# Optimization experiments

Measured on AMD Instinct MI355X. Metric: run time of the kernel, lower is better.

The kernel has to match this reference:

```python
import jax, jax.numpy as jnp
import numpy as np
import math

B_, V_, D_, N_, H_, W_ = 4, 8, 64, 16, 32, 32
V_LIST = [0.0, 45.0, 90.0, 135.0, 180.0, 225.0, 270.0, 315.0]
GROUPS = 4
EPS = 1e-5


def _make_sample_coords():
    # Replicates F.affine_grid(align_corners=False) for fixed rotation matrices,
    # then maps normalized grid coords to input pixel coords as grid_sample does.
    xs = (np.arange(W_) + 0.5) * 2.0 / W_ - 1.0
    ys = (np.arange(H_) + 0.5) * 2.0 / H_ - 1.0
    X, Y = np.meshgrid(xs, ys)  # (H, W)
    ix_list, iy_list = [], []
    for w in V_LIST:
        a = math.radians(-w)
        c, s = math.cos(a), math.sin(a)
        gx = c * X - s * Y  # theta = [[c,-s,0],[s,c,0]]
        gy = s * X + c * Y
        ix_list.append((gx + 1.0) * W_ / 2.0 - 0.5)
        iy_list.append((gy + 1.0) * H_ / 2.0 - 0.5)
    return (jnp.asarray(np.stack(ix_list), jnp.float32),
            jnp.asarray(np.stack(iy_list), jnp.float32))

IX, IY = _make_sample_coords()  # each (V, H, W)


def _bilinear(sv, iy, ix):
    # sv: (B, D, N, H, W); iy, ix: (H, W) float sampling coords (pixel space)
    x0 = jnp.floor(ix)
    y0 = jnp.floor(iy)
    wx1 = ix - x0
    wy1 = iy - y0

    def corner(yc, xc, wgt):
        m = (yc >= 0) & (yc < H_) & (xc >= 0) & (xc < W_)  # zeros padding
        yi = jnp.clip(yc, 0, H_ - 1).astype(jnp.int32)
        xi = jnp.clip(xc, 0, W_ - 1).astype(jnp.int32)
        return sv[..., yi, xi] * jnp.where(m, wgt, 0.0)

    return (corner(y0, x0, (1.0 - wy1) * (1.0 - wx1))
            + corner(y0, x0 + 1.0, (1.0 - wy1) * wx1)
            + corner(y0 + 1.0, x0, wy1 * (1.0 - wx1))
            + corner(y0 + 1.0, x0 + 1.0, wy1 * wx1))

# vmap over the velocity axis V of s_prev and the per-velocity grids
_transport = jax.vmap(_bilinear, in_axes=(1, 0, 0), out_axes=1)


def _conv(x, w, b=None):
    y = jax.lax.conv_general_dilated(x, w, (1, 1), 'SAME',
                                     dimension_numbers=('NCHW', 'OIHW', 'NCHW'))
    if b is not None:
        y = y + b[None, :, None, None]
    return y


def _group_norm(x, w, b):
    Bn, D, H, W = x.shape
    xg = x.reshape(Bn, GROUPS, D // GROUPS, H, W)
    mu = xg.mean(axis=(2, 3, 4), keepdims=True)
    var = xg.var(axis=(2, 3, 4), keepdims=True)
    xn = ((xg - mu) * jax.lax.rsqrt(var + EPS)).reshape(Bn, D, H, W)
    return xn * w[None, :, None, None] + b[None, :, None, None]


def setup_inputs() -> dict:
    key = jax.random.key(0)
    ks = jax.random.split(key, 5)
    return {
        "u_t": jax.random.normal(ks[0], (B_, D_, H_, W_), jnp.float32),
        "s_prev": jax.random.normal(ks[1], (B_, V_, D_, N_, H_, W_), jnp.float32) * 0.1,
        "gn_w": jnp.ones((D_,), jnp.float32),
        "gn_b": jnp.zeros((D_,), jnp.float32),
        "conv_delta_w": jax.random.normal(ks[2], (D_, D_, 3, 3), jnp.float32) * 0.02,
        "conv_delta_b": jnp.zeros((D_,), jnp.float32),
        "conv_B_w": jax.random.normal(ks[3], (N_, D_, 3, 3), jnp.float32) * 0.02,
        "conv_C_w": jax.random.normal(ks[4], (N_, D_, 3, 3), jnp.float32) * 0.02,
        "log_A_real": jnp.full((D_, N_), math.log(0.5), jnp.float32),
        "D_param": jnp.ones((D_,), jnp.float32),
        "dt_bias": jnp.float32(math.log(math.e - 1.0)),
    }


def reference(u_t, s_prev, gn_w, gn_b, conv_delta_w, conv_delta_b,
              conv_B_w, conv_C_w, log_A_real, D_param, dt_bias):
    u_norm = _group_norm(u_t, gn_w, gn_b)
    delta = jax.nn.softplus(_conv(u_norm, conv_delta_w, conv_delta_b) + dt_bias)
    delta = jnp.clip(delta, 1e-4, 5.0)                               # (B,D,H,W)
    B_val = _conv(u_norm, conv_B_w)                                  # (B,N,H,W)
    C_val = _conv(u_norm, conv_C_w)                                  # (B,N,H,W)
    A = -jnp.exp(log_A_real)                                         # (D,N)
    A_bar = jnp.exp(delta[:, :, None] * A[None, :, :, None, None])   # (B,D,N,H,W)
    B_bar = delta[:, :, None] * B_val[:, None]                       # (B,D,N,H,W)
    s_trans = _transport(s_prev, IY, IX)                             # (B,V,D,N,H,W)
    s_new = A_bar[:, None] * s_trans + B_bar[:, None] * u_t[:, None, :, None]
    y_state = jnp.einsum('bvdnhw,bnhw->bvdhw', s_new, C_val)
    y_new = y_state + u_t[:, None] * D_param[None, None, :, None, None]
    return (y_new, s_new)
```

## Files before the change

kernel.cpp:

```cpp
#include <hip/hip_runtime.h>
#include <cmath>

#define FSQ 0.70710678118654752440f
__constant__ float CTAB[8] = {1.f,  FSQ, 0.f, -FSQ, -1.f, -FSQ, 0.f, FSQ};
__constant__ float STAB[8] = {0.f, -FSQ, -1.f, -FSQ,  0.f,  FSQ, 1.f, FSQ};

__global__ __launch_bounds__(256) void gn_kernel(const float* __restrict__ u,
                                                 const float* __restrict__ gw,
                                                 const float* __restrict__ gb,
                                                 float* __restrict__ up)
{
    int blk = blockIdx.x;
    int b = blk >> 2, g = blk & 3;
    int t = threadIdx.x;
    const float* src = u + ((size_t)(b * 64 + g * 16) << 10);
    float sum = 0.f, sq = 0.f;
    #pragma unroll
    for (int r = 0; r < 64; ++r) {
        float v = src[t + (r << 8)];
        sum += v; sq += v * v;
    }
    __shared__ float red[256], red2[256];
    red[t] = sum; red2[t] = sq;
    __syncthreads();
    for (int ofs = 128; ofs > 0; ofs >>= 1) {
        if (t < ofs) { red[t] += red[t + ofs]; red2[t] += red2[t + ofs]; }
        __syncthreads();
    }
    float mu  = red[0] * (1.f / 16384.f);
    float var = red2[0] * (1.f / 16384.f) - mu * mu;
    float rs  = rsqrtf(var + 1e-5f);

    float* pb = up + (size_t)(b * 64 + g * 16) * 1156;
    for (int k = t; k < 16 * 132; k += 256) {
        int pl = k / 132, c = k % 132;
        int idx;
        if (c < 34)       idx = c;
        else if (c < 68)  idx = 33 * 34 + (c - 34);
        else if (c < 100) idx = (c - 68 + 1) * 34;
        else              idx = (c - 100 + 1) * 34 + 33;
        pb[pl * 1156 + idx] = 0.f;
    }
    for (int r = 0; r < 64; ++r) {
        int idx = t + (r << 8);
        int ch = idx >> 10, rem = idx & 1023;
        int y = rem >> 5, x = rem & 31;
        float val = (src[idx] - mu) * rs * gw[g * 16 + ch] + gb[g * 16 + ch];
        pb[ch * 1156 + (y + 1) * 34 + (x + 1)] = val;
    }
}

__global__ __launch_bounds__(256) void conv_kernel(const float* __restrict__ up,
                                                   const float* __restrict__ wd,
                                                   const float* __restrict__ bd,
                                                   const float* __restrict__ wB,
                                                   const float* __restrict__ wC,
                                                   const float* __restrict__ dtb,
                                                   float* __restrict__ delta,
                                                   float* __restrict__ Bv,
                                                   float* __restrict__ Cv)
{
    __shared__ float sin_[64 * 204];
    __shared__ float red[256];
    int blk = blockIdx.x;
    int strip = blk & 7;
    int o = (blk >> 3) & 127; o = o % 96;
    o = ((blk >> 3) - (blk / 768) * 96);
    int b = blk / 768;
    int h0 = strip * 4;
    int t = threadIdx.x;

    const float* plane = up + (size_t)b * 73984;
    for (int idx = t; idx < 13056; idx += 256) {
        int ci = idx / 204;
        int rem = idx - ci * 204;
        sin_[idx] = plane[ci * 1156 + h0 * 34 + rem];
    }
    __syncthreads();

    const float* wsel;
    if (o < 64)      wsel = wd + (size_t)o * 576;
    else if (o < 80) wsel = wB + (size_t)(o - 64) * 576;
    else             wsel = wC + (size_t)(o - 80) * 576;

    int half = t >> 7;
    int px = t & 127;
    int r = px >> 5, c = px & 31;
    const float* base = sin_ + r * 34 + c;

    float acc = 0.f;
    int ci0 = half * 32;
    for (int ci = ci0; ci < ci0 + 32; ++ci) {
        const float* pp = base + ci * 204;
        const float* wp = wsel + ci * 9;
        #pragma unroll
        for (int dy = 0; dy < 3; ++dy)
            #pragma unroll
            for (int dx = 0; dx < 3; ++dx)
                acc += pp[dy * 34 + dx] * wp[dy * 3 + dx];
    }
    red[t] = acc;
    __syncthreads();
    if (t < 128) {
        float a = red[t] + red[t + 128];
        int pidx = (h0 + r) * 32 + c;
        if (o < 64) {
            float x = a + bd[o] + dtb[0];
            float sp = (x > 20.f) ? x : log1pf(expf(x));
            sp = fminf(fmaxf(sp, 1e-4f), 5.f);
            delta[((size_t)(b * 64 + o) << 10) + pidx] = sp;
        } else if (o < 80) {
            Bv[((size_t)(b * 16 + o - 64) << 10) + pidx] = a;
        } else {
            Cv[((size_t)(b * 16 + o - 80) << 10) + pidx] = a;
        }
    }
}

__global__ __launch_bounds__(256) void fused_state_kernel(
    const float* __restrict__ s_prev, const float* __restrict__ u_t,
    const float* __restrict__ delta, const float* __restrict__ Bv,
    const float* __restrict__ Cv, const float* __restrict__ logA,
    const float* __restrict__ Dp, float* __restrict__ y_out,
    float* __restrict__ s_out)
{
    __shared__ float lds[8 * 1156];
    __shared__ float Ash[8];
    int blk = blockIdx.x;
    int cchunk = blk & 1;
    int d = (blk >> 1) & 63, v = (blk >> 7) & 7, b = blk >> 10;
    int t = threadIdx.x;

    if (t < 8) Ash[t] = -__expf(logA[d * 16 + cchunk * 8 + t]);
    for (int k = t; k < 1056; k += 256) {
        int pl = k >> 7; int g = k & 127;
        pl = k / 132; g = k - pl * 132;
        int idx;
        if (g < 34)       idx = g;
        else if (g < 68)  idx = 1122 + (g - 34);
        else if (g < 100) idx = (g - 67) * 34;
        else              idx = (g - 99) * 34 + 33;
        lds[pl * 1156 + idx] = 0.f;
    }

    size_t so = (((size_t)((b * 8 + v) * 64 + d)) << 14) + (cchunk << 13);
    const float4* src = (const float4*)(s_prev + so);
    #pragma unroll
    for (int k = 0; k < 8; ++k) {
        int q = t + (k << 8);
        float4 val = src[q];
        int lin = q << 2;
        int nn = lin >> 10, rem = lin & 1023;
        int di = nn * 1156 + ((rem >> 5) + 1) * 34 + (rem & 31) + 1;
        lds[di] = val.x; lds[di + 1] = val.y; lds[di + 2] = val.z; lds[di + 3] = val.w;
    }
    __syncthreads();

    const float cc = CTAB[v], ss = STAB[v];
    const float* dpl = delta + ((size_t)(b * 64 + d) << 10);
    const float* upl = u_t   + ((size_t)(b * 64 + d) << 10);
    const float* bvc = Bv + ((size_t)b << 14) + (cchunk << 13);
    const float* cvc = Cv + ((size_t)b << 14) + (cchunk << 13);
    float* soc = s_out + so;
    float* yo  = y_out + (((size_t)((b * 8 + v) * 64 + d)) << 10);
    float Dd = Dp[d];

    for (int i = 0; i < 4; ++i) {
        int p = t + (i << 8);
        int h = p >> 5, wpx = p & 31;
        float X = (wpx + 0.5f) * 0.0625f - 1.f;
        float Y = (h + 0.5f) * 0.0625f - 1.f;
        float gx = cc * X - ss * Y;
        float gy = ss * X + cc * Y;
        float ix = (gx + 1.f) * 16.f - 0.5f;
        float iy = (gy + 1.f) * 16.f - 0.5f;
        float fx0 = floorf(ix), fy0 = floorf(iy);
        float wx = ix - fx0, wy = iy - fy0;
        int x0 = (int)fx0, y0 = (int)fy0;
        float mx0 = (x0 >= 0 && x0 < 32) ? (1.f - wx) : 0.f;
        float mx1 = (x0 >= -1 && x0 < 31) ? wx : 0.f;
        float my0 = (y0 >= 0 && y0 < 32) ? (1.f - wy) : 0.f;
        float my1 = (y0 >= -1 && y0 < 31) ? wy : 0.f;
        float w00 = my0 * mx0, w01 = my0 * mx1;
        float w10 = my1 * mx0, w11 = my1 * mx1;
        int bx = min(max(x0, -1), 31), by = min(max(y0, -1), 31);
        int base = (by + 1) * 34 + (bx + 1);

        float dd = dpl[p], uv = upl[p];
        float du = dd * uv;
        float yacc = 0.f;
        #pragma unroll
        for (int nn = 0; nn < 8; ++nn) {
            int si = base + nn * 1156;
            float s00 = lds[si], s01 = lds[si + 1];
            float s10 = lds[si + 34], s11 = lds[si + 35];
            float bil = s00 * w00 + s01 * w01 + s10 * w10 + s11 * w11;
            float abar = __expf(dd * Ash[nn]);
            float bvv = bvc[(nn << 10) + p];
            float sn = abar * bil + du * bvv;
            soc[(nn << 10) + p] = sn;
            yacc += sn * cvc[(nn << 10) + p];
        }
        float val = yacc + (cchunk == 0 ? uv * Dd : 0.f);
        atomicAdd(yo + p, val);
    }
}

extern "C" void kernel_launch(void* const* d_in, const int* in_sizes, int n_in,
                              void* d_out, int out_size, void* d_ws, size_t ws_size,
                              hipStream_t stream)
{
    const float* u_t    = (const float*)d_in[0];
    const float* s_prev = (const float*)d_in[1];
    const float* gn_w   = (const float*)d_in[2];
    const float* gn_b   = (const float*)d_in[3];
    const float* wd     = (const float*)d_in[4];
    const float* bd     = (const float*)d_in[5];
    const float* wB     = (const float*)d_in[6];
    const float* wC     = (const float*)d_in[7];
    const float* logA   = (const float*)d_in[8];
    const float* Dp     = (const float*)d_in[9];
    const float* dtb    = (const float*)d_in[10];

    float* y_out = (float*)d_out;
    float* s_out = y_out + 2097152;

    float* up    = (float*)d_ws;
    float* delta = up + 295936;
    float* Bv    = delta + 262144;
    float* Cv    = Bv + 65536;

    hipMemsetAsync(y_out, 0, (size_t)2097152 * sizeof(float), stream);

    hipLaunchKernelGGL(gn_kernel, dim3(16), dim3(256), 0, stream, u_t, gn_w, gn_b, up);
    hipLaunchKernelGGL(conv_kernel, dim3(3072), dim3(256), 0, stream,
                       up, wd, bd, wB, wC, dtb, delta, Bv, Cv);
    hipLaunchKernelGGL(fused_state_kernel, dim3(4096), dim3(256), 0, stream,
                       s_prev, u_t, delta, Bv, Cv, logA, Dp, y_out, s_out);
}
```

Before: 319.3 us.

## Specialize transport for right-angle rotations, drop atomics and memset

The fused state kernel now handles all 16 state channels per block, so y is written directly with float4 stores instead of atomicAdd, and the output memset is removed. Rotations by 0 and 180 degrees read s_prev straight from global memory with index remapping, skipping LDS staging. Rotations by 90 and 270 degrees use a single exact gather instead of bilinear interpolation. Odd-angle views keep bilinear sampling, process 4 pixels per thread and stage two 8-channel chunks through LDS. The costs are more register pressure and branch specialisation per view, and the right-angle paths rely on the fixed angle list being exact.

```diff
diff --git a/kernel.cpp b/kernel.cpp
--- a/kernel.cpp
+++ b/kernel.cpp
@@ -64,9 +64,8 @@
     __shared__ float red[256];
     int blk = blockIdx.x;
     int strip = blk & 7;
-    int o = (blk >> 3) & 127; o = o % 96;
-    o = ((blk >> 3) - (blk / 768) * 96);
     int b = blk / 768;
+    int o = (blk >> 3) - b * 96;
     int h0 = strip * 4;
     int t = threadIdx.x;
 
@@ -125,85 +124,148 @@
     float* __restrict__ s_out)
 {
     __shared__ float lds[8 * 1156];
-    __shared__ float Ash[8];
+    __shared__ float Ash[16];
     int blk = blockIdx.x;
-    int cchunk = blk & 1;
-    int d = (blk >> 1) & 63, v = (blk >> 7) & 7, b = blk >> 10;
+    int d = blk & 63, v = (blk >> 6) & 7, b = blk >> 9;
     int t = threadIdx.x;
 
-    if (t < 8) Ash[t] = -__expf(logA[d * 16 + cchunk * 8 + t]);
-    for (int k = t; k < 1056; k += 256) {
-        int pl = k >> 7; int g = k & 127;
-        pl = k / 132; g = k - pl * 132;
-        int idx;
-        if (g < 34)       idx = g;
-        else if (g < 68)  idx = 1122 + (g - 34);
-        else if (g < 100) idx = (g - 67) * 34;
-        else              idx = (g - 99) * 34 + 33;
-        lds[pl * 1156 + idx] = 0.f;
-    }
-
-    size_t so = (((size_t)((b * 8 + v) * 64 + d)) << 14) + (cchunk << 13);
-    const float4* src = (const float4*)(s_prev + so);
-    #pragma unroll
-    for (int k = 0; k < 8; ++k) {
-        int q = t + (k << 8);
-        float4 val = src[q];
-        int lin = q << 2;
-        int nn = lin >> 10, rem = lin & 1023;
-        int di = nn * 1156 + ((rem >> 5) + 1) * 34 + (rem & 31) + 1;
-        lds[di] = val.x; lds[di + 1] = val.y; lds[di + 2] = val.z; lds[di + 3] = val.w;
+    int h = t >> 3;
+    int x = (t & 7) << 2;
+
+    if (t < 16) Ash[t] = -__expf(logA[d * 16 + t]);
+
+    bool is_odd = (v & 1);
+    if (is_odd) {
+        for (int k = t; k < 1056; k += 256) {
+            int pl = k / 132, g = k - pl * 132;
+            int idx;
+            if (g < 34)       idx = g;
+            else if (g < 68)  idx = 1122 + (g - 34);
+            else if (g < 100) idx = (g - 67) * 34;
+            else              idx = (g - 99) * 34 + 33;
+            lds[pl * 1156 + idx] = 0.f;
+        }
     }
     __syncthreads();
 
-    const float cc = CTAB[v], ss = STAB[v];
-    const float* dpl = delta + ((size_t)(b * 64 + d) << 10);
-    const float* upl = u_t   + ((size_t)(b * 64 + d) << 10);
-    const float* bvc = Bv + ((size_t)b << 14) + (cchunk << 13);
-    const float* cvc = Cv + ((size_t)b << 14) + (cchunk << 13);
-    float* soc = s_out + so;
-    float* yo  = y_out + (((size_t)((b * 8 + v) * 64 + d)) << 10);
+    size_t so = ((size_t)((b * 8 + v) * 64 + d)) << 14;
+    const float*  sb   = s_prev + so;
+    float*        sob  = s_out + so;
+    const float4* dpl4 = (const float4*)(delta + ((size_t)(b * 64 + d) << 10));
+    const float4* upl4 = (const float4*)(u_t   + ((size_t)(b * 64 + d) << 10));
+    const float4* Bv4  = (const float4*)(Bv + ((size_t)b << 14));
+    const float4* Cv4  = (const float4*)(Cv + ((size_t)b << 14));
+    float4*       sot4 = (float4*)sob;
+    float4*       yo4  = (float4*)(y_out + (((size_t)((b * 8 + v) * 64 + d)) << 10));
+
+    float4 dl = dpl4[t];
+    float4 uu = upl4[t];
+    float4 du = make_float4(dl.x * uu.x, dl.y * uu.y, dl.z * uu.z, dl.w * uu.w);
+    float4 yacc = make_float4(0.f, 0.f, 0.f, 0.f);
+
+    if (v == 0 || v == 4) {
+        const float4* sp4 = (const float4*)sb;
+        int rd = (v == 0) ? t : (((31 - h) << 3) + ((28 - x) >> 2));
+        #pragma unroll
+        for (int nn = 0; nn < 16; ++nn) {
+            float4 sp = sp4[(nn << 8) + rd];
+            float s0, s1, s2, s3;
+            if (v == 0) { s0 = sp.x; s1 = sp.y; s2 = sp.z; s3 = sp.w; }
+            else        { s0 = sp.w; s1 = sp.z; s2 = sp.y; s3 = sp.x; }
+            float A = Ash[nn];
+            float4 bv = Bv4[(nn << 8) + t];
+            float4 cv = Cv4[(nn << 8) + t];
+            float4 sn;
+            sn.x = __expf(dl.x * A) * s0 + du.x * bv.x;
+            sn.y = __expf(dl.y * A) * s1 + du.y * bv.y;
+            sn.z = __expf(dl.z * A) * s2 + du.z * bv.z;
+            sn.w = __expf(dl.w * A) * s3 + du.w * bv.w;
+            sot4[(nn << 8) + t] = sn;
+            yacc.x += sn.x * cv.x; yacc.y += sn.y * cv.y;
+            yacc.z += sn.z * cv.z; yacc.w += sn.w * cv.w;
+        }
+    } else {
+        int base0[4];
+        float w00[4], w01[4], w10[4], w11[4];
+        if (is_odd) {
+            const float cc = CTAB[v], ss = STAB[v];
+            #pragma unroll
+            for (int j = 0; j < 4; ++j) {
+                float X = (x + j + 0.5f) * 0.0625f - 1.f;
+                float Y = (h + 0.5f) * 0.0625f - 1.f;
+                float gx = cc * X - ss * Y;
+                float gy = ss * X + cc * Y;
+                float ix = (gx + 1.f) * 16.f - 0.5f;
+                float iy = (gy + 1.f) * 16.f - 0.5f;
+                float fx0 = floorf(ix), fy0 = floorf(iy);
+                float wx = ix - fx0, wy = iy - fy0;
+                int x0 = (int)fx0, y0 = (int)fy0;
+                float mx0 = (x0 >= 0 && x0 < 32) ? (1.f - wx) : 0.f;
+                float mx1 = (x0 >= -1 && x0 < 31) ? wx : 0.f;
+                float my0 = (y0 >= 0 && y0 < 32) ? (1.f - wy) : 0.f;
+                float my1 = (y0 >= -1 && y0 < 31) ? wy : 0.f;
+                w00[j] = my0 * mx0; w01[j] = my0 * mx1;
+                w10[j] = my1 * mx0; w11[j] = my1 * mx1;
+                int bx = min(max(x0, -1), 31), by = min(max(y0, -1), 31);
+                base0[j] = (by + 1) * 34 + (bx + 1);
+            }
+        } else {
+            #pragma unroll
+            for (int j = 0; j < 4; ++j) {
+                if (v == 2) base0[j] = (32 - x - j) * 34 + (h + 1);
+                else        base0[j] = (x + j + 1) * 34 + (32 - h);
+            }
+        }
+
+        for (int ch = 0; ch < 2; ++ch) {
+            const float* src = sb + (ch << 13);
+            #pragma unroll
+            for (int k = 0; k < 32; ++k) {
+                int idx = t + (k << 8);
+                int nn = idx >> 10, rem = idx & 1023;
+                lds[nn * 1156 + ((rem >> 5) + 1) * 34 + (rem & 31) + 1] = src[idx];
+            }
+            __syncthreads();
+
+            #pragma unroll
+            for (int n = 0; n < 8; ++n) {
+                int nn = (ch << 3) + n;
+                float A = Ash[nn];
+                float4 bv = Bv4[(nn << 8) + t];
+                float4 cv = Cv4[(nn << 8) + t];
+                float bil[4];
+                if (is_odd) {
+                    #pragma unroll
+                    for (int j = 0; j < 4; ++j) {
+                        int si = base0[j] + n * 1156;
+                        bil[j] = lds[si] * w00[j] + lds[si + 1] * w01[j]
+                               + lds[si + 34] * w10[j] + lds[si + 35] * w11[j];
+                    }
+                } else {
+                    #pragma unroll
+                    for (int j = 0; j < 4; ++j)
+                        bil[j] = lds[base0[j] + n * 1156];
+                }
+                float4 sn;
+                sn.x = __expf(dl.x * A) * bil[0] + du.x * bv.x;
+                sn.y = __expf(dl.y * A) * bil[1] + du.y * bv.y;
+                sn.z = __expf(dl.z * A) * bil[2] + du.z * bv.z;
+                sn.w = __expf(dl.w * A) * bil[3] + du.w * bv.w;
+                sot4[(nn << 8) + t] = sn;
+                yacc.x += sn.x * cv.x; yacc.y += sn.y * cv.y;
+                yacc.z += sn.z * cv.z; yacc.w += sn.w * cv.w;
+            }
+            __syncthreads();
+        }
+    }
+
     float Dd = Dp[d];
-
-    for (int i = 0; i < 4; ++i) {
-        int p = t + (i << 8);
-        int h = p >> 5, wpx = p & 31;
-        float X = (wpx + 0.5f) * 0.0625f - 1.f;
-        float Y = (h + 0.5f) * 0.0625f - 1.f;
-        float gx = cc * X - ss * Y;
-        float gy = ss * X + cc * Y;
-        float ix = (gx + 1.f) * 16.f - 0.5f;
-        float iy = (gy + 1.f) * 16.f - 0.5f;
-        float fx0 = floorf(ix), fy0 = floorf(iy);
-        float wx = ix - fx0, wy = iy - fy0;
-        int x0 = (int)fx0, y0 = (int)fy0;
-        float mx0 = (x0 >= 0 && x0 < 32) ? (1.f - wx) : 0.f;
-        float mx1 = (x0 >= -1 && x0 < 31) ? wx : 0.f;
-        float my0 = (y0 >= 0 && y0 < 32) ? (1.f - wy) : 0.f;
-        float my1 = (y0 >= -1 && y0 < 31) ? wy : 0.f;
-        float w00 = my0 * mx0, w01 = my0 * mx1;
-        float w10 = my1 * mx0, w11 = my1 * mx1;
-        int bx = min(max(x0, -1), 31), by = min(max(y0, -1), 31);
-        int base = (by + 1) * 34 + (bx + 1);
-
-        float dd = dpl[p], uv = upl[p];
-        float du = dd * uv;
-        float yacc = 0.f;
-        #pragma unroll
-        for (int nn = 0; nn < 8; ++nn) {
-            int si = base + nn * 1156;
-            float s00 = lds[si], s01 = lds[si + 1];
-            float s10 = lds[si + 34], s11 = lds[si + 35];
-            float bil = s00 * w00 + s01 * w01 + s10 * w10 + s11 * w11;
-            float abar = __expf(dd * Ash[nn]);
-            float bvv = bvc[(nn << 10) + p];
-            float sn = abar * bil + du * bvv;
-            soc[(nn << 10) + p] = sn;
-            yacc += sn * cvc[(nn << 10) + p];
-        }
-        float val = yacc + (cchunk == 0 ? uv * Dd : 0.f);
-        atomicAdd(yo + p, val);
-    }
+    float4 y4;
+    y4.x = yacc.x + uu.x * Dd;
+    y4.y = yacc.y + uu.y * Dd;
+    y4.z = yacc.z + uu.z * Dd;
+    y4.w = yacc.w + uu.w * Dd;
+    yo4[t] = y4;
 }
 
 extern "C" void kernel_launch(void* const* d_in, const int* in_sizes, int n_in,
@@ -230,11 +292,9 @@
     float* Bv    = delta + 262144;
     float* Cv    = Bv + 65536;
 
-    hipMemsetAsync(y_out, 0, (size_t)2097152 * sizeof(float), stream);
-
     hipLaunchKernelGGL(gn_kernel, dim3(16), dim3(256), 0, stream, u_t, gn_w, gn_b, up);
     hipLaunchKernelGGL(conv_kernel, dim3(3072), dim3(256), 0, stream,
                        up, wd, bd, wB, wC, dtb, delta, Bv, Cv);
-    hipLaunchKernelGGL(fused_state_kernel, dim3(4096), dim3(256), 0, stream,
+    hipLaunchKernelGGL(fused_state_kernel, dim3(2048), dim3(256), 0, stream,
                        s_prev, u_t, delta, Bv, Cv, logA, Dp, y_out, s_out);
 }
```

Measured after the change: 324.1 us. About the same (+1.5%).
